# Kernel tuning notes

Hardware: AMD Instinct MI355X
Metric: run time of the kernel (lower is better)

## Reference

```python
import jax, jax.numpy as jnp
import numpy as np

N, E, D = 40000, 320000, 128          # nodes, edges, model dim
H, C = 4, 128                          # GAT heads, per-head channels
DEPTH, MLP = 2, 512
NEG_SLOPE = 0.2
EPS_SM = 1e-16                         # PyG softmax denom epsilon


def layer_norm(x, g, b):
    mu = jnp.mean(x, axis=-1, keepdims=True)
    var = jnp.var(x, axis=-1, keepdims=True)
    return (x - mu) * jax.lax.rsqrt(var + 1e-5) * g + b


def gat_conv(x, src, dst, edge_attr, W, a_src, a_dst, We, a_edge, bias):
    # x: [N,D]; W: [D,H*C]; a_*: [H,C]; We: [1,H*C]; bias: [H*C]
    h = (x @ W).reshape(N, H, C)                       # [N,H,C]
    alpha_src = jnp.einsum('nhc,hc->nh', h, a_src)      # [N,H]
    alpha_dst = jnp.einsum('nhc,hc->nh', h, a_dst)      # [N,H]
    e = (edge_attr @ We).reshape(E, H, C)               # [E,H,C]
    alpha_e = jnp.einsum('ehc,hc->eh', e, a_edge)       # [E,H]
    alpha = alpha_src[src] + alpha_dst[dst] + alpha_e   # [E,H]
    alpha = jax.nn.leaky_relu(alpha, NEG_SLOPE)
    # segment softmax over edges sharing the same destination node
    amax = jax.ops.segment_max(alpha, dst, num_segments=N)   # [N,H]
    ex = jnp.exp(alpha - amax[dst])                          # [E,H]
    denom = jax.ops.segment_sum(ex, dst, num_segments=N)     # [N,H]
    attn = ex / (denom[dst] + EPS_SM)                        # [E,H]
    # message = attn * x_j ; aggregate by destination (scatter-add)
    msg = attn[:, :, None] * h[src]                          # [E,H,C]
    out = jax.ops.segment_sum(msg, dst, num_segments=N)      # [N,H,C]
    return out.reshape(N, H * C) + bias                      # concat heads


def setup_inputs():
    key = jax.random.key(0)
    ks = jax.random.split(key, 16)
    s = 0.05
    f32 = jnp.float32
    inp = {
        'x': jax.random.normal(ks[0], (N, D), f32),
        'edge_index': jax.random.randint(ks[1], (2, E), 0, N),
        'edge_attr': jax.random.normal(ks[2], (E, 1), f32),
        'ln1_g': jnp.ones((DEPTH, D), f32),
        'ln1_b': jnp.zeros((DEPTH, D), f32),
        'gat_W': jax.random.normal(ks[3], (DEPTH, D, H * C), f32) * s,
        'att_src': jax.random.normal(ks[4], (DEPTH, H, C), f32) * s,
        'att_dst': jax.random.normal(ks[5], (DEPTH, H, C), f32) * s,
        'edge_W': jax.random.normal(ks[6], (DEPTH, 1, H * C), f32) * s,
        'att_edge': jax.random.normal(ks[7], (DEPTH, H, C), f32) * s,
        'gat_bias': jnp.zeros((DEPTH, H * C), f32),
        'qf_W': jax.random.normal(ks[8], (DEPTH, H * C, D), f32) * s,
        'qf_b': jnp.zeros((DEPTH, D), f32),
        'ln2_g': jnp.ones((DEPTH, D), f32),
        'ln2_b': jnp.zeros((DEPTH, D), f32),
        'ff_W1': jax.random.normal(ks[9], (DEPTH, D, MLP), f32) * s,
        'ff_b1': jnp.zeros((DEPTH, MLP), f32),
        'ff_W2': jax.random.normal(ks[10], (DEPTH, MLP, D), f32) * s,
        'ff_b2': jnp.zeros((DEPTH, D), f32),
    }
    return inp


def reference(x, edge_index, edge_attr, ln1_g, ln1_b, gat_W, att_src, att_dst,
              edge_W, att_edge, gat_bias, qf_W, qf_b, ln2_g, ln2_b,
              ff_W1, ff_b1, ff_W2, ff_b2):
    src, dst = edge_index[0], edge_index[1]
    for d in range(DEPTH):
        # Residual(PreNorm(QuickFix(GATConv)))
        h = layer_norm(x, ln1_g[d], ln1_b[d])
        g = gat_conv(h, src, dst, edge_attr, gat_W[d], att_src[d], att_dst[d],
                     edge_W[d], att_edge[d], gat_bias[d])
        x = x + g @ qf_W[d] + qf_b[d]
        # Residual(PreNorm(FeedForward))
        h = layer_norm(x, ln2_g[d], ln2_b[d])
        x = x + jax.nn.gelu(h @ ff_W1[d] + ff_b1[d]) @ ff_W2[d] + ff_b2[d]
    return x
```

## Files before the change

### kernel.cpp

```cpp
#include <hip/hip_runtime.h>
#include <hip/hip_bf16.h>

#define N_NODES 40000
#define N_EDGES 320000
#define DIM 128
#define HC 512
#define NHEAD 4
#define CHEAD 128
#define DEPTH_L 2
#define MLP_DIM 512
#define SCAN_NB ((N_NODES + 255) / 256)

typedef __attribute__((ext_vector_type(8))) short short8;
typedef __attribute__((ext_vector_type(4))) float f32x4;

static __device__ __forceinline__ void gload_lds16(const void* g, void* l)
{
    __builtin_amdgcn_global_load_lds(
        (const __attribute__((address_space(1))) unsigned int*)g,
        (__attribute__((address_space(3))) unsigned int*)l,
        16, 0, 0);
}

static __device__ __forceinline__ unsigned int packbf2(float a, float b)
{
    union { __hip_bfloat16 h[2]; unsigned int u; } p;
    p.h[0] = __float2bfloat16(a);
    p.h[1] = __float2bfloat16(b);
    return p.u;
}

static __device__ __forceinline__ float gelu_f(float v)
{
    float z2 = -1.5957691216f * (v + 0.044715f * v * v * v);
    return v / (1.f + __expf(z2));
}

struct PrepArgs {
    const float* wsrc[4];
    __hip_bfloat16* wdst[4];
    int wK[4];
    int wN[4];
    const float* gat_W;
    const float* att_src;
    const float* att_dst;
    const float* edge_W;
    const float* att_edge;
    const float* gat_bias;
    const float* qf_W;
    const float* qf_b;
    float* uvec;
    __hip_bfloat16* Mt;
    float* cvec;
    float* ae;
};
__global__ __launch_bounds__(256) void k_prep(PrepArgs a)
{
    int b = blockIdx.x;
    int tid = threadIdx.x;
    if (b < 1024) {
        int j = b >> 8;
        int i = (b & 255) * 256 + tid;
        int K = a.wK[j], N = a.wN[j];
        if (i < K * N) {
            int n = i / K, k = i % K;
            a.wdst[j][i] = __float2bfloat16(a.wsrc[j][(size_t)k * N + n]);
        }
    } else if (b < 1040) {
        if (tid < 128) {
            int bb = b - 1024;
            int d = bb >> 3, t8 = bb & 7;
            int t = t8 >> 2, h = t8 & 3;
            int c = tid;
            const float* W = a.gat_W + (size_t)d * DIM * HC;
            const float* av = (t == 0 ? a.att_src : a.att_dst)
                              + (size_t)d * NHEAD * CHEAD + h * CHEAD;
            float s = 0.f;
            for (int cc = 0; cc < CHEAD; ++cc)
                s += W[(size_t)c * HC + h * CHEAD + cc] * av[cc];
            a.uvec[(size_t)d * 1024 + t8 * 128 + c] = s;
        }
    } else if (b < 1552) {
        int i = (b - 1040) * 256 + tid;
        int d = i >> 16;
        int hk = (i >> 7) & 511;
        int j = i & 127;
        int h = hk >> 7, k = hk & 127;
        const float* W = a.gat_W + (size_t)d * DIM * HC + (size_t)k * HC + h * CHEAD;
        const float* Q = a.qf_W + (size_t)d * HC * DIM + (size_t)h * CHEAD * DIM + j;
        float s = 0.f;
        for (int c = 0; c < CHEAD; ++c)
            s += W[c] * Q[(size_t)c * DIM];
        a.Mt[(size_t)d * 65536 + (size_t)j * 512 + hk] = __float2bfloat16(s);
    } else if (b < 1616) {
        int idx = (b - 1552) * 4 + (tid >> 6);
        int lane = tid & 63;
        int d = idx >> 7, j = idx & 127;
        float s = 0.f;
        for (int m = lane; m < HC; m += 64)
            s += a.gat_bias[(size_t)d * HC + m]
               * a.qf_W[(size_t)d * HC * DIM + (size_t)m * DIM + j];
        #pragma unroll
        for (int dd = 32; dd; dd >>= 1) s += __shfl_xor(s, dd);
        if (lane == 0) a.cvec[idx] = s + a.qf_b[(size_t)d * DIM + j];
    } else {
        int d = b - 1616;
        int h = tid >> 6, lane = tid & 63;
        float2 w = *reinterpret_cast<const float2*>(
            a.edge_W + (size_t)d * HC + h * CHEAD + lane * 2);
        float2 av = *reinterpret_cast<const float2*>(
            a.att_edge + (size_t)d * NHEAD * CHEAD + h * CHEAD + lane * 2);
        float s = w.x * av.x + w.y * av.y;
        #pragma unroll
        for (int dd = 32; dd; dd >>= 1) s += __shfl_xor(s, dd);
        if (lane == 0) a.ae[d * 4 + h] = s;
    }
}

__global__ void k_hist(const int* __restrict__ dst, int* __restrict__ deg)
{
    int e = blockIdx.x * 256 + threadIdx.x;
    if (e < N_EDGES) atomicAdd(&deg[dst[e]], 1);
}

__global__ __launch_bounds__(256) void k_scan1(const int* __restrict__ deg,
                                               int* __restrict__ off,
                                               int* __restrict__ bsum)
{
    __shared__ int wsum[4];
    int b = blockIdx.x;
    int t = threadIdx.x, lane = t & 63, w = t >> 6;
    int i = b * 256 + t;
    int v = (i < N_NODES) ? deg[i] : 0;
    int s = v;
    #pragma unroll
    for (int d = 1; d < 64; d <<= 1) {
        int u = __shfl_up(s, d);
        if (lane >= d) s += u;
    }
    if (lane == 63) wsum[w] = s;
    __syncthreads();
    int wpre = 0;
    #pragma unroll
    for (int j = 0; j < 4; ++j)
        if (j < w) wpre += wsum[j];
    if (i < N_NODES) off[i] = wpre + s - v;
    if (t == 255) bsum[b] = wpre + s;
}

__global__ __launch_bounds__(256) void k_scan2(int* __restrict__ bsum,
                                               int* __restrict__ bpre)
{
    __shared__ int wsum[4];
    int t = threadIdx.x, lane = t & 63, w = t >> 6;
    int v = (t < SCAN_NB) ? bsum[t] : 0;
    int s = v;
    #pragma unroll
    for (int d = 1; d < 64; d <<= 1) {
        int u = __shfl_up(s, d);
        if (lane >= d) s += u;
    }
    if (lane == 63) wsum[w] = s;
    __syncthreads();
    int wpre = 0;
    #pragma unroll
    for (int j = 0; j < 4; ++j)
        if (j < w) wpre += wsum[j];
    if (t < SCAN_NB) bpre[t] = wpre + s - v;
    if (t == 255) bpre[SCAN_NB] = wpre + s;
}

__global__ __launch_bounds__(256) void k_scan3(int* __restrict__ off,
                                               const int* __restrict__ bpre,
                                               int* __restrict__ cur)
{
    int b = blockIdx.x;
    int i = b * 256 + threadIdx.x;
    if (i < N_NODES) {
        int o = off[i] + bpre[b];
        off[i] = o;
        cur[i] = o;
    }
    if (i == 0) off[N_NODES] = bpre[SCAN_NB];
}

__global__ void k_fill(const int* __restrict__ src, const int* __restrict__ dst,
                       const float* __restrict__ ea, int* __restrict__ cur,
                       int* __restrict__ scsr, int* __restrict__ dcsr,
                       float* __restrict__ eacsr)
{
    int e = blockIdx.x * 256 + threadIdx.x;
    if (e < N_EDGES) {
        int dd = dst[e];
        int p = atomicAdd(&cur[dd], 1);
        scsr[p] = src[e];
        dcsr[p] = dd;
        eacsr[p] = ea[e];
    }
}

__global__ __launch_bounds__(256) void k_ln(const float* __restrict__ x,
                                            const float* __restrict__ gma,
                                            const float* __restrict__ bta,
                                            const float* __restrict__ uvec,
                                            __hip_bfloat16* __restrict__ out,
                                            float* __restrict__ asrc,
                                            float* __restrict__ adst, int M)
{
    int row = blockIdx.x * 4 + (threadIdx.x >> 6);
    int lane = threadIdx.x & 63;
    if (row >= M) return;
    float2 v = *reinterpret_cast<const float2*>(x + (size_t)row * DIM + lane * 2);
    float s = v.x + v.y, sq = v.x * v.x + v.y * v.y;
    #pragma unroll
    for (int d = 32; d; d >>= 1) { s += __shfl_xor(s, d); sq += __shfl_xor(sq, d); }
    float mean = s * (1.f / DIM);
    float var = sq * (1.f / DIM) - mean * mean;
    float rs = rsqrtf(var + 1e-5f);
    int c = lane * 2;
    float h0 = (v.x - mean) * rs * gma[c] + bta[c];
    float h1 = (v.y - mean) * rs * gma[c + 1] + bta[c + 1];
    *reinterpret_cast<unsigned int*>(out + (size_t)row * DIM + c) = packbf2(h0, h1);
    float ss[8];
    #pragma unroll
    for (int tt = 0; tt < 8; ++tt) {
        float2 uv = *reinterpret_cast<const float2*>(uvec + tt * 128 + c);
        ss[tt] = h0 * uv.x + h1 * uv.y;
    }
    #pragma unroll
    for (int d = 32; d; d >>= 1) {
        #pragma unroll
        for (int tt = 0; tt < 8; ++tt) ss[tt] += __shfl_xor(ss[tt], d);
    }
    if (lane == 0) {
        reinterpret_cast<float4*>(asrc)[row] = make_float4(ss[0], ss[1], ss[2], ss[3]);
        reinterpret_cast<float4*>(adst)[row] = make_float4(ss[4], ss[5], ss[6], ss[7]);
    }
}

__global__ __launch_bounds__(256) void k_alpha(const int* __restrict__ scsr,
                                               const int* __restrict__ dcsr,
                                               const float* __restrict__ eacsr,
                                               const float* __restrict__ asrc,
                                               const float* __restrict__ adst,
                                               const float* __restrict__ ae4v,
                                               float* __restrict__ wcsr)
{
    int p = blockIdx.x * 256 + threadIdx.x;
    if (p >= N_EDGES) return;
    int s = scsr[p], dd = dcsr[p];
    float q = eacsr[p];
    float4 as = reinterpret_cast<const float4*>(asrc)[s];
    float4 ad = reinterpret_cast<const float4*>(adst)[dd];
    float4 ae = *reinterpret_cast<const float4*>(ae4v);
    float4 w;
    float al;
    al = as.x + ad.x + ae.x * q; al = al > 0.f ? al : 0.2f * al; w.x = __expf(al);
    al = as.y + ad.y + ae.y * q; al = al > 0.f ? al : 0.2f * al; w.y = __expf(al);
    al = as.z + ad.z + ae.z * q; al = al > 0.f ? al : 0.2f * al; w.z = __expf(al);
    al = as.w + ad.w + ae.w * q; al = al > 0.f ? al : 0.2f * al; w.w = __expf(al);
    reinterpret_cast<float4*>(wcsr)[p] = w;
}

__global__ __launch_bounds__(256) void k_agg2(const int* __restrict__ off,
                                              const int* __restrict__ scsr,
                                              const float* __restrict__ wcsr,
                                              const unsigned int* __restrict__ hln,
                                              unsigned int* __restrict__ agg)
{
    int n = blockIdx.x * 4 + (threadIdx.x >> 6);
    int lane = threadIdx.x & 63;
    int e0 = off[n], e1 = off[n + 1];
    float den[4] = {0, 0, 0, 0};
    float accA[4] = {0, 0, 0, 0};
    float accB[4] = {0, 0, 0, 0};
    int i = e0;
    for (; i + 3 < e1; i += 4) {
        int s0 = scsr[i], s1 = scsr[i + 1], s2 = scsr[i + 2], s3 = scsr[i + 3];
        float4 w0 = reinterpret_cast<const float4*>(wcsr)[i];
        float4 w1 = reinterpret_cast<const float4*>(wcsr)[i + 1];
        float4 w2 = reinterpret_cast<const float4*>(wcsr)[i + 2];
        float4 w3 = reinterpret_cast<const float4*>(wcsr)[i + 3];
        unsigned int u0 = hln[s0 * 64 + lane];
        unsigned int u1 = hln[s1 * 64 + lane];
        unsigned int u2 = hln[s2 * 64 + lane];
        unsigned int u3 = hln[s3 * 64 + lane];
        float f00 = __uint_as_float(u0 << 16), f01 = __uint_as_float(u0 & 0xffff0000u);
        float f10 = __uint_as_float(u1 << 16), f11 = __uint_as_float(u1 & 0xffff0000u);
        float f20 = __uint_as_float(u2 << 16), f21 = __uint_as_float(u2 & 0xffff0000u);
        float f30 = __uint_as_float(u3 << 16), f31 = __uint_as_float(u3 & 0xffff0000u);
        den[0] += (w0.x + w1.x) + (w2.x + w3.x);
        den[1] += (w0.y + w1.y) + (w2.y + w3.y);
        den[2] += (w0.z + w1.z) + (w2.z + w3.z);
        den[3] += (w0.w + w1.w) + (w2.w + w3.w);
        accA[0] += w0.x * f00 + w1.x * f10 + w2.x * f20 + w3.x * f30;
        accB[0] += w0.x * f01 + w1.x * f11 + w2.x * f21 + w3.x * f31;
        accA[1] += w0.y * f00 + w1.y * f10 + w2.y * f20 + w3.y * f30;
        accB[1] += w0.y * f01 + w1.y * f11 + w2.y * f21 + w3.y * f31;
        accA[2] += w0.z * f00 + w1.z * f10 + w2.z * f20 + w3.z * f30;
        accB[2] += w0.z * f01 + w1.z * f11 + w2.z * f21 + w3.z * f31;
        accA[3] += w0.w * f00 + w1.w * f10 + w2.w * f20 + w3.w * f30;
        accB[3] += w0.w * f01 + w1.w * f11 + w2.w * f21 + w3.w * f31;
    }
    for (; i < e1; ++i) {
        int s0 = scsr[i];
        float4 w0 = reinterpret_cast<const float4*>(wcsr)[i];
        unsigned int u0 = hln[s0 * 64 + lane];
        float f00 = __uint_as_float(u0 << 16);
        float f01 = __uint_as_float(u0 & 0xffff0000u);
        den[0] += w0.x; den[1] += w0.y; den[2] += w0.z; den[3] += w0.w;
        accA[0] += w0.x * f00; accB[0] += w0.x * f01;
        accA[1] += w0.y * f00; accB[1] += w0.y * f01;
        accA[2] += w0.z * f00; accB[2] += w0.z * f01;
        accA[3] += w0.w * f00; accB[3] += w0.w * f01;
    }
    #pragma unroll
    for (int h = 0; h < 4; ++h) {
        float inv = 1.f / (den[h] + 1e-16f);
        agg[n * 256 + h * 64 + lane] = packbf2(accA[h] * inv, accB[h] * inv);
    }
}

template <bool LN>
__global__ __launch_bounds__(256) void k_qf(const short* __restrict__ A,
                                            const short* __restrict__ Bt,
                                            const float* __restrict__ bias,
                                            const float* __restrict__ resid,
                                            float* __restrict__ xout,
                                            const float* __restrict__ gma,
                                            const float* __restrict__ bta,
                                            __hip_bfloat16* __restrict__ hout,
                                            int M)
{
    __shared__ __align__(16) short Bls[2][128 * 64];
    const int tid = threadIdx.x;
    const int lane = tid & 63;
    const int w = tid >> 6;
    const int lrow = lane & 15;
    const int lk = lane >> 4;
    const int mw = blockIdx.x * 64 + w * 16;

    short8 aq[16];
    #pragma unroll
    for (int t = 0; t < 16; ++t)
        aq[t] = *reinterpret_cast<const short8*>(
            A + (size_t)(mw + lrow) * 512 + t * 32 + lk * 8);

    auto stage = [&](int buf, int kt) {
        #pragma unroll
        for (int c0 = 0; c0 < 1024; c0 += 256) {
            int c = c0 + tid;
            int wb = c0 + (w << 6);
            int r = c >> 3, gq = c & 7, gp = gq ^ (r & 7);
            gload_lds16(Bt + (size_t)r * 512 + kt + gp * 8, &Bls[buf][wb * 8]);
        }
    };

    f32x4 acc[8] = {};
    stage(0, 0);
    __syncthreads();
    int cur = 0;
    for (int t = 0; t < 8; ++t) {
        if (t < 7) stage(cur ^ 1, (t + 1) * 64);
        #pragma unroll
        for (int ks = 0; ks < 2; ++ks) {
            short8 af = aq[t * 2 + ks];
            short8 bf[8];
            #pragma unroll
            for (int fj = 0; fj < 8; ++fj) {
                int r = fj * 16 + lrow;
                int g = ks * 4 + lk;
                bf[fj] = *reinterpret_cast<const short8*>(
                    &Bls[cur][r * 64 + ((g ^ (r & 7)) * 8)]);
            }
            #pragma unroll
            for (int fj = 0; fj < 8; ++fj)
                acc[fj] = __builtin_amdgcn_mfma_f32_16x16x32_bf16(
                    af, bf[fj], acc[fj], 0, 0, 0);
        }
        __syncthreads();
        cur ^= 1;
    }

    #pragma unroll
    for (int p = 0; p < 4; ++p) {
        int m = mw + lk * 4 + p;
        float v[8], s = 0.f, sq = 0.f;
        #pragma unroll
        for (int fj = 0; fj < 8; ++fj) {
            int n = fj * 16 + lrow;
            v[fj] = acc[fj][p] + bias[n] + resid[(size_t)m * DIM + n];
            s += v[fj]; sq += v[fj] * v[fj];
        }
        #pragma unroll
        for (int fj = 0; fj < 8; ++fj)
            xout[(size_t)m * DIM + fj * 16 + lrow] = v[fj];
        if (LN) {
            #pragma unroll
            for (int d = 1; d < 16; d <<= 1) {
                s += __shfl_xor(s, d);
                sq += __shfl_xor(sq, d);
            }
            float mean = s * (1.f / DIM);
            float var = sq * (1.f / DIM) - mean * mean;
            float rs = rsqrtf(var + 1e-5f);
            #pragma unroll
            for (int fj = 0; fj < 8; ++fj) {
                int n = fj * 16 + lrow;
                hout[(size_t)m * DIM + n] =
                    __float2bfloat16((v[fj] - mean) * rs * gma[n] + bta[n]);
            }
        }
    }
}

template <bool LNN>
__global__ __launch_bounds__(256) void k_ff(const short* __restrict__ A,
                                            const short* __restrict__ W1t,
                                            const short* __restrict__ W2t,
                                            const float* __restrict__ b1,
                                            const float* __restrict__ b2,
                                            const float* __restrict__ resid,
                                            float* __restrict__ xout,
                                            const float* __restrict__ gma,
                                            const float* __restrict__ bta,
                                            __hip_bfloat16* __restrict__ hout,
                                            const float* __restrict__ uvec,
                                            float* __restrict__ asrcO,
                                            float* __restrict__ adstO,
                                            int M)
{
    __shared__ __align__(16) short B1ls[64 * 128];
    __shared__ __align__(16) short B2ls[128 * 64];
    __shared__ __align__(16) short midls[4][16 * 64];
    const int tid = threadIdx.x;
    const int lane = tid & 63;
    const int w = tid >> 6;
    const int lrow = lane & 15;
    const int lk = lane >> 4;
    const int mw = blockIdx.x * 64 + w * 16;
    __hip_bfloat16* midw = (__hip_bfloat16*)midls[w];

    short8 af[4];
    #pragma unroll
    for (int ks = 0; ks < 4; ++ks)
        af[ks] = *reinterpret_cast<const short8*>(
            A + (size_t)(mw + lrow) * 128 + ks * 32 + lk * 8);

    auto stage1 = [&](int mc) {
        #pragma unroll
        for (int c0 = 0; c0 < 1024; c0 += 256) {
            int c = c0 + tid;
            int wb = c0 + (w << 6);
            int r = c >> 4, gq = c & 15, gp = gq ^ (r & 15);
            gload_lds16(W1t + (size_t)(mc * 64 + r) * 128 + gp * 8, &B1ls[wb * 8]);
        }
    };
    auto stage2 = [&](int mc) {
        #pragma unroll
        for (int c0 = 0; c0 < 1024; c0 += 256) {
            int c = c0 + tid;
            int wb = c0 + (w << 6);
            int r = c >> 3, gq = c & 7, gp = gq ^ (r & 7);
            gload_lds16(W2t + (size_t)r * 512 + mc * 64 + gp * 8, &B2ls[wb * 8]);
        }
    };

    f32x4 acc2[8] = {};
    stage1(0);
    for (int mc = 0; mc < 8; ++mc) {
        __syncthreads();
        stage2(mc);
        f32x4 acc1[4] = {};
        #pragma unroll
        for (int ks = 0; ks < 4; ++ks) {
            short8 bf1[4];
            #pragma unroll
            for (int fj = 0; fj < 4; ++fj) {
                int r = fj * 16 + lrow;
                bf1[fj] = *reinterpret_cast<const short8*>(
                    &B1ls[r * 128 + (((ks * 4 + lk) ^ (r & 15)) * 8)]);
            }
            #pragma unroll
            for (int fj = 0; fj < 4; ++fj)
                acc1[fj] = __builtin_amdgcn_mfma_f32_16x16x32_bf16(
                    af[ks], bf1[fj], acc1[fj], 0, 0, 0);
        }
        #pragma unroll
        for (int fj = 0; fj < 4; ++fj) {
            #pragma unroll
            for (int p = 0; p < 4; ++p) {
                int mloc = lk * 4 + p;
                int cloc = fj * 16 + lrow;
                float v = gelu_f(acc1[fj][p] + b1[mc * 64 + cloc]);
                int slot = (cloc >> 3) ^ (mloc & 7);
                midw[mloc * 64 + slot * 8 + (cloc & 7)] = __float2bfloat16(v);
            }
        }
        __syncthreads();
        if (mc < 7) stage1(mc + 1);
        #pragma unroll
        for (int ks2 = 0; ks2 < 2; ++ks2) {
            int g = ks2 * 4 + lk;
            short8 a2 = *reinterpret_cast<const short8*>(
                &midls[w][lrow * 64 + ((g ^ (lrow & 7)) * 8)]);
            short8 bf2[8];
            #pragma unroll
            for (int fj = 0; fj < 8; ++fj) {
                int r = fj * 16 + lrow;
                bf2[fj] = *reinterpret_cast<const short8*>(
                    &B2ls[r * 64 + ((g ^ (r & 7)) * 8)]);
            }
            #pragma unroll
            for (int fj = 0; fj < 8; ++fj)
                acc2[fj] = __builtin_amdgcn_mfma_f32_16x16x32_bf16(
                    a2, bf2[fj], acc2[fj], 0, 0, 0);
        }
    }

    float uvv[8][8];
    if (LNN) {
        #pragma unroll
        for (int tt = 0; tt < 8; ++tt)
            #pragma unroll
            for (int fj = 0; fj < 8; ++fj)
                uvv[tt][fj] = uvec[tt * 128 + fj * 16 + lrow];
    }

    #pragma unroll
    for (int p = 0; p < 4; ++p) {
        int m = mw + lk * 4 + p;
        float v[8], s = 0.f, sq = 0.f;
        #pragma unroll
        for (int fj = 0; fj < 8; ++fj) {
            int n = fj * 16 + lrow;
            v[fj] = acc2[fj][p] + b2[n] + resid[(size_t)m * DIM + n];
            s += v[fj]; sq += v[fj] * v[fj];
        }
        #pragma unroll
        for (int fj = 0; fj < 8; ++fj)
            xout[(size_t)m * DIM + fj * 16 + lrow] = v[fj];
        if (LNN) {
            #pragma unroll
            for (int d = 1; d < 16; d <<= 1) {
                s += __shfl_xor(s, d);
                sq += __shfl_xor(sq, d);
            }
            float mean = s * (1.f / DIM);
            float var = sq * (1.f / DIM) - mean * mean;
            float rs = rsqrtf(var + 1e-5f);
            float ss[8] = {0, 0, 0, 0, 0, 0, 0, 0};
            #pragma unroll
            for (int fj = 0; fj < 8; ++fj) {
                int n = fj * 16 + lrow;
                float h = (v[fj] - mean) * rs * gma[n] + bta[n];
                hout[(size_t)m * DIM + n] = __float2bfloat16(h);
                #pragma unroll
                for (int tt = 0; tt < 8; ++tt) ss[tt] += h * uvv[tt][fj];
            }
            #pragma unroll
            for (int d = 1; d < 16; d <<= 1) {
                #pragma unroll
                for (int tt = 0; tt < 8; ++tt) ss[tt] += __shfl_xor(ss[tt], d);
            }
            if (lrow == 0) {
                reinterpret_cast<float4*>(asrcO)[m] =
                    make_float4(ss[0], ss[1], ss[2], ss[3]);
                reinterpret_cast<float4*>(adstO)[m] =
                    make_float4(ss[4], ss[5], ss[6], ss[7]);
            }
        }
    }
}

extern "C" void kernel_launch(void* const* d_in, const int* in_sizes, int n_in,
                              void* d_out, int out_size, void* d_ws, size_t ws_size,
                              hipStream_t stream)
{
    const float* x_in     = (const float*)d_in[0];
    const int*   ei       = (const int*)d_in[1];
    const float* ea       = (const float*)d_in[2];
    const float* ln1_g    = (const float*)d_in[3];
    const float* ln1_b    = (const float*)d_in[4];
    const float* gat_W    = (const float*)d_in[5];
    const float* att_src  = (const float*)d_in[6];
    const float* att_dst  = (const float*)d_in[7];
    const float* edge_W   = (const float*)d_in[8];
    const float* att_edge = (const float*)d_in[9];
    const float* gat_bias = (const float*)d_in[10];
    const float* qf_W     = (const float*)d_in[11];
    const float* qf_b     = (const float*)d_in[12];
    const float* ln2_g    = (const float*)d_in[13];
    const float* ln2_b    = (const float*)d_in[14];
    const float* ff_W1    = (const float*)d_in[15];
    const float* ff_b1    = (const float*)d_in[16];
    const float* ff_W2    = (const float*)d_in[17];
    const float* ff_b2    = (const float*)d_in[18];
    float* x = (float*)d_out;

    char* ws = (char*)d_ws;
    size_t o = 0;
    auto alloc = [&](size_t b) { size_t r = o; o += (b + 255) & ~(size_t)255; return r; };
    __hip_bfloat16*  h_ln  = (__hip_bfloat16*)(ws + alloc((size_t)N_NODES * DIM * 2));
    __hip_bfloat16*  gbuf  = (__hip_bfloat16*)(ws + alloc((size_t)N_NODES * HC * 2));
    float*           asrc  = (float*)(ws + alloc((size_t)N_NODES * 4 * 4));
    float*           adst  = (float*)(ws + alloc((size_t)N_NODES * 4 * 4));
    float*           ae4   = (float*)(ws + alloc(256));
    float*           uvec  = (float*)(ws + alloc((size_t)DEPTH_L * 1024 * 4));
    __hip_bfloat16*  Mt    = (__hip_bfloat16*)(ws + alloc((size_t)DEPTH_L * 65536 * 2));
    float*           cvec  = (float*)(ws + alloc(256 * 4));
    int*             deg   = (int*)(ws + alloc((size_t)(N_NODES + 1) * 4));
    int*             off   = (int*)(ws + alloc((size_t)(N_NODES + 1) * 4));
    int*             cur   = (int*)(ws + alloc((size_t)N_NODES * 4));
    int*             bsum  = (int*)(ws + alloc((size_t)(SCAN_NB + 1) * 4));
    int*             bpre  = (int*)(ws + alloc((size_t)(SCAN_NB + 1) * 4));
    int*             scsr  = (int*)(ws + alloc((size_t)N_EDGES * 4));
    int*             dcsr  = (int*)(ws + alloc((size_t)N_EDGES * 4));
    float*           eacsr = (float*)(ws + alloc((size_t)N_EDGES * 4));
    float*           wcsr  = (float*)(ws + alloc((size_t)N_EDGES * 4 * 4));
    __hip_bfloat16* Wt[DEPTH_L][2];
    for (int d = 0; d < DEPTH_L; ++d)
        for (int j = 0; j < 2; ++j)
            Wt[d][j] = (__hip_bfloat16*)(ws + alloc((size_t)65536 * 2));

    const int* srcA = ei;
    const int* dstA = ei + N_EDGES;

    PrepArgs pa;
    for (int d = 0; d < DEPTH_L; ++d) {
        pa.wsrc[d * 2 + 0] = ff_W1 + (size_t)d * DIM * MLP_DIM;
        pa.wK[d * 2 + 0] = DIM;     pa.wN[d * 2 + 0] = MLP_DIM;
        pa.wsrc[d * 2 + 1] = ff_W2 + (size_t)d * MLP_DIM * DIM;
        pa.wK[d * 2 + 1] = MLP_DIM; pa.wN[d * 2 + 1] = DIM;
        pa.wdst[d * 2 + 0] = Wt[d][0];
        pa.wdst[d * 2 + 1] = Wt[d][1];
    }
    pa.gat_W = gat_W; pa.att_src = att_src; pa.att_dst = att_dst;
    pa.edge_W = edge_W; pa.att_edge = att_edge;
    pa.gat_bias = gat_bias; pa.qf_W = qf_W; pa.qf_b = qf_b;
    pa.uvec = uvec; pa.Mt = Mt; pa.cvec = cvec; pa.ae = ae4;
    k_prep<<<1618, 256, 0, stream>>>(pa);

    hipMemsetAsync(deg, 0, (size_t)(N_NODES + 1) * 4, stream);
    k_hist<<<(N_EDGES + 255) / 256, 256, 0, stream>>>(dstA, deg);
    k_scan1<<<SCAN_NB, 256, 0, stream>>>(deg, off, bsum);
    k_scan2<<<1, 256, 0, stream>>>(bsum, bpre);
    k_scan3<<<SCAN_NB, 256, 0, stream>>>(off, bpre, cur);
    k_fill<<<(N_EDGES + 255) / 256, 256, 0, stream>>>(srcA, dstA, ea, cur, scsr, dcsr, eacsr);

    const int QB = N_NODES / 64;
    const int NB = N_NODES / 4;
    const int EB = (N_EDGES + 255) / 256;

    k_ln<<<NB, 256, 0, stream>>>(x_in, ln1_g, ln1_b, uvec, h_ln, asrc, adst, N_NODES);

    for (int d = 0; d < DEPTH_L; ++d) {
        const float* resid0 = (d == 0) ? x_in : x;
        k_alpha<<<EB, 256, 0, stream>>>(scsr, dcsr, eacsr, asrc, adst, ae4 + d * 4, wcsr);
        k_agg2<<<NB, 256, 0, stream>>>(off, scsr, wcsr, (const unsigned int*)h_ln,
            (unsigned int*)gbuf);
        k_qf<true><<<QB, 256, 0, stream>>>((const short*)gbuf,
            (const short*)(Mt + (size_t)d * 65536), cvec + d * 128, resid0, x,
            ln2_g + d * DIM, ln2_b + d * DIM, h_ln, N_NODES);
        if (d + 1 < DEPTH_L) {
            k_ff<true><<<QB, 256, 0, stream>>>((const short*)h_ln,
                (const short*)Wt[d][0], (const short*)Wt[d][1],
                ff_b1 + d * MLP_DIM, ff_b2 + d * DIM, x, x,
                ln1_g + (d + 1) * DIM, ln1_b + (d + 1) * DIM, h_ln,
                uvec + (size_t)(d + 1) * 1024, asrc, adst, N_NODES);
        } else {
            k_ff<false><<<QB, 256, 0, stream>>>((const short*)h_ln,
                (const short*)Wt[d][0], (const short*)Wt[d][1],
                ff_b1 + d * MLP_DIM, ff_b2 + d * DIM, x, x,
                nullptr, nullptr, nullptr,
                nullptr, nullptr, nullptr, N_NODES);
        }
    }
}
```

Measured before the change: 261.8 us.

## Double-buffer FFN weight tiles and transpose MFMA to pack GELU stores

The fused feed-forward kernel now keeps two LDS buffers each for the W1 and W2 tiles and prefetches chunk mc+1 while computing chunk mc, which removes the mid-loop barrier that used to guard the W1 reload. The first-stage MFMA operands are swapped so each lane holds four consecutive output columns, which lets the GELU results be packed into one 8-byte LDS store instead of four scalar bf16 stores. LDS use roughly doubles for the weight tiles, which can lower occupancy. Dropping the second barrier relies on the per-wave mid buffer being read only by the wave that wrote it.

```diff
diff --git a/kernel.cpp b/kernel.cpp
--- a/kernel.cpp
+++ b/kernel.cpp
@@ -430,8 +430,8 @@
                                             float* __restrict__ adstO,
                                             int M)
 {
-    __shared__ __align__(16) short B1ls[64 * 128];
-    __shared__ __align__(16) short B2ls[128 * 64];
+    __shared__ __align__(16) short B1ls[2][64 * 128];
+    __shared__ __align__(16) short B2ls[2][128 * 64];
     __shared__ __align__(16) short midls[4][16 * 64];
     const int tid = threadIdx.x;
     const int lane = tid & 63;
@@ -439,7 +439,7 @@
     const int lrow = lane & 15;
     const int lk = lane >> 4;
     const int mw = blockIdx.x * 64 + w * 16;
-    __hip_bfloat16* midw = (__hip_bfloat16*)midls[w];
+    short* midw = midls[w];
 
     short8 af[4];
     #pragma unroll
@@ -447,30 +447,34 @@
         af[ks] = *reinterpret_cast<const short8*>(
             A + (size_t)(mw + lrow) * 128 + ks * 32 + lk * 8);
 
-    auto stage1 = [&](int mc) {
+    auto stage1 = [&](int buf, int mc) {
         #pragma unroll
         for (int c0 = 0; c0 < 1024; c0 += 256) {
             int c = c0 + tid;
             int wb = c0 + (w << 6);
             int r = c >> 4, gq = c & 15, gp = gq ^ (r & 15);
-            gload_lds16(W1t + (size_t)(mc * 64 + r) * 128 + gp * 8, &B1ls[wb * 8]);
+            gload_lds16(W1t + (size_t)(mc * 64 + r) * 128 + gp * 8,
+                        &B1ls[buf][wb * 8]);
         }
     };
-    auto stage2 = [&](int mc) {
+    auto stage2 = [&](int buf, int mc) {
         #pragma unroll
         for (int c0 = 0; c0 < 1024; c0 += 256) {
             int c = c0 + tid;
             int wb = c0 + (w << 6);
             int r = c >> 3, gq = c & 7, gp = gq ^ (r & 7);
-            gload_lds16(W2t + (size_t)r * 512 + mc * 64 + gp * 8, &B2ls[wb * 8]);
+            gload_lds16(W2t + (size_t)r * 512 + mc * 64 + gp * 8,
+                        &B2ls[buf][wb * 8]);
         }
     };
 
     f32x4 acc2[8] = {};
-    stage1(0);
+    stage1(0, 0);
+    stage2(0, 0);
     for (int mc = 0; mc < 8; ++mc) {
+        const int buf = mc & 1;
         __syncthreads();
-        stage2(mc);
+        if (mc < 7) { stage1(buf ^ 1, mc + 1); stage2(buf ^ 1, mc + 1); }
         f32x4 acc1[4] = {};
         #pragma unroll
         for (int ks = 0; ks < 4; ++ks) {
@@ -479,37 +483,38 @@
             for (int fj = 0; fj < 4; ++fj) {
                 int r = fj * 16 + lrow;
                 bf1[fj] = *reinterpret_cast<const short8*>(
-                    &B1ls[r * 128 + (((ks * 4 + lk) ^ (r & 15)) * 8)]);
+                    &B1ls[buf][r * 128 + (((ks * 4 + lk) ^ (r & 15)) * 8)]);
             }
             #pragma unroll
             for (int fj = 0; fj < 4; ++fj)
                 acc1[fj] = __builtin_amdgcn_mfma_f32_16x16x32_bf16(
-                    af[ks], bf1[fj], acc1[fj], 0, 0, 0);
+                    bf1[fj], af[ks], acc1[fj], 0, 0, 0);
         }
         #pragma unroll
         for (int fj = 0; fj < 4; ++fj) {
-            #pragma unroll
-            for (int p = 0; p < 4; ++p) {
-                int mloc = lk * 4 + p;
-                int cloc = fj * 16 + lrow;
-                float v = gelu_f(acc1[fj][p] + b1[mc * 64 + cloc]);
-                int slot = (cloc >> 3) ^ (mloc & 7);
-                midw[mloc * 64 + slot * 8 + (cloc & 7)] = __float2bfloat16(v);
-            }
-        }
-        __syncthreads();
-        if (mc < 7) stage1(mc + 1);
+            int cb = fj * 16 + lk * 4;
+            float v0 = gelu_f(acc1[fj][0] + b1[mc * 64 + cb + 0]);
+            float v1 = gelu_f(acc1[fj][1] + b1[mc * 64 + cb + 1]);
+            float v2 = gelu_f(acc1[fj][2] + b1[mc * 64 + cb + 2]);
+            float v3 = gelu_f(acc1[fj][3] + b1[mc * 64 + cb + 3]);
+            int gw = cb >> 3;
+            int addr = lrow * 64 + ((gw ^ (lrow & 7)) * 8) + (lk & 1) * 4;
+            uint2 pk;
+            pk.x = packbf2(v0, v1);
+            pk.y = packbf2(v2, v3);
+            *reinterpret_cast<uint2*>(&midw[addr]) = pk;
+        }
         #pragma unroll
         for (int ks2 = 0; ks2 < 2; ++ks2) {
             int g = ks2 * 4 + lk;
             short8 a2 = *reinterpret_cast<const short8*>(
-                &midls[w][lrow * 64 + ((g ^ (lrow & 7)) * 8)]);
+                &midw[lrow * 64 + ((g ^ (lrow & 7)) * 8)]);
             short8 bf2[8];
             #pragma unroll
             for (int fj = 0; fj < 8; ++fj) {
                 int r = fj * 16 + lrow;
                 bf2[fj] = *reinterpret_cast<const short8*>(
-                    &B2ls[r * 64 + ((g ^ (r & 7)) * 8)]);
+                    &B2ls[buf][r * 64 + ((g ^ (r & 7)) * 8)]);
             }
             #pragma unroll
             for (int fj = 0; fj < 8; ++fj)
```

Result: no change. 265.8 us (+1.6%).
